# Optimization experiments

Measured on AMD Instinct MI355X. Metric: run time of the kernel, lower is better.

The kernel has to match this reference:

```python
import jax, jax.numpy as jnp
import numpy as np

B, T, N, F = 32, 36, 10000, 3
HORIZON = 10
NUM_REGIONS = 20
NAN_RATE = 0.05


def setup_inputs() -> dict:
    key = jax.random.key(0)
    k1, k2, k3 = jax.random.split(key, 3)
    seq = jax.random.normal(k1, (B, T, N, F), dtype=jnp.float32)
    nan_mask = jax.random.uniform(k2, (B, T, N, F)) < NAN_RATE
    seq = jnp.where(nan_mask, jnp.nan, seq)
    cluster_id = jax.random.randint(k3, (N,), 0, NUM_REGIONS, dtype=jnp.int64)
    return {"seq": seq, "cluster_id": cluster_id}


def _nanmean_all(x):
    valid = ~jnp.isnan(x)
    s = jnp.where(valid, x, 0.0).sum()
    c = valid.sum().astype(x.dtype)
    return s / c


def reference(seq, cluster_id):
    x = seq[..., 0]                               # [B, T, N] speed channel
    valid = ~jnp.isnan(x)
    xz = jnp.where(valid, x, 0.0)
    cnt = valid.sum(axis=1).astype(x.dtype)       # [B, N]
    time_mean = xz.sum(axis=1) / cnt              # [B, N]; NaN if a node is all-NaN
    pred_speed = jnp.tile(time_mean[:, None, :], (1, HORIZON, 1))  # [B, 10, N]

    # per-region nanmean over nodes: segment-mean via one-hot contraction
    onehot = (cluster_id[:, None] == jnp.arange(NUM_REGIONS)).astype(x.dtype)  # [N, R]
    pvalid = ~jnp.isnan(pred_speed)
    pz = jnp.where(pvalid, pred_speed, 0.0)
    rsum = jnp.einsum('bhn,nr->bhr', pz, onehot)                     # [B, 10, R]
    rcnt = jnp.einsum('bhn,nr->bhr', pvalid.astype(x.dtype), onehot)  # [B, 10, R]
    regional = rsum / rcnt                                            # NaN if region all-NaN

    # nan_to_global_avg: replace remaining NaNs with global nanmean of each tensor
    g1 = _nanmean_all(pred_speed)
    g2 = _nanmean_all(regional)
    out_pred = jnp.where(jnp.isnan(pred_speed), g1, pred_speed)
    out_regional = jnp.where(jnp.isnan(regional), g2, regional)
    return out_pred, out_regional
```

## Files before the change

kernel.cpp:

```cpp
#include <hip/hip_runtime.h>

#define BB 32
#define TT 36
#define NN 10000
#define FF 3
#define HH 10
#define RR 20
#define NQ (NN / 4)


__global__ __launch_bounds__(256) void k_time_mean(
        const float* __restrict__ seq,
        const int* __restrict__ cid,
        float* __restrict__ tm,
        float* __restrict__ rsum,
        float* __restrict__ rcnt) {
    __shared__ float ls[RR];
    __shared__ float lc[RR];
    const int b = blockIdx.y;
    const int q = blockIdx.x * blockDim.x + threadIdx.x;
    if (threadIdx.x < RR) { ls[threadIdx.x] = 0.f; lc[threadIdx.x] = 0.f; }
    __syncthreads();

    if (q < NQ) {
        const float4* p = (const float4*)seq + (size_t)b * TT * NN * FF / 4 + 3 * q;
        const size_t tstride = (size_t)NN * FF / 4;
        float s0 = 0.f, s1 = 0.f, s2 = 0.f, s3 = 0.f;
        int c0 = 0, c1 = 0, c2 = 0, c3 = 0;
        #pragma unroll
        for (int t = 0; t < TT; ++t) {
            float4 q0 = p[0];
            float4 q1 = p[1];
            float4 q2 = p[2];
            p += tstride;
            float v0 = q0.x, v1 = q0.w, v2 = q1.z, v3 = q2.y;
            if (v0 == v0) { s0 += v0; c0++; }
            if (v1 == v1) { s1 += v1; c1++; }
            if (v2 == v2) { s2 += v2; c2++; }
            if (v3 == v3) { s3 += v3; c3++; }
        }
        const float nanf_ = __int_as_float(0x7fc00000);
        float m0 = c0 ? s0 / (float)c0 : nanf_;
        float m1 = c1 ? s1 / (float)c1 : nanf_;
        float m2 = c2 ? s2 / (float)c2 : nanf_;
        float m3 = c3 ? s3 / (float)c3 : nanf_;
        ((float4*)tm)[(size_t)b * NQ + q] = make_float4(m0, m1, m2, m3);

        const int4 r4 = ((const int4*)cid)[q];
        if (c0) { atomicAdd(&ls[r4.x], m0); atomicAdd(&lc[r4.x], 1.f); }
        if (c1) { atomicAdd(&ls[r4.y], m1); atomicAdd(&lc[r4.y], 1.f); }
        if (c2) { atomicAdd(&ls[r4.z], m2); atomicAdd(&lc[r4.z], 1.f); }
        if (c3) { atomicAdd(&ls[r4.w], m3); atomicAdd(&lc[r4.w], 1.f); }
    }

    __syncthreads();
    if (threadIdx.x < RR) {
        atomicAdd(&rsum[b * RR + threadIdx.x], ls[threadIdx.x]);
        atomicAdd(&rcnt[b * RR + threadIdx.x], lc[threadIdx.x]);
    }
}

__global__ void k_regional(const float* __restrict__ rsum,
                           const float* __restrict__ rcnt,
                           float* __restrict__ g1out,
                           float* __restrict__ out_reg) {
    const int tid = threadIdx.x;
    __shared__ float sv[10], sc[10], ss[10], sn[10];
    __shared__ float g2s;

    float myrs = 0.f, myrc = 0.f;
    float val = 0.f;
    int valid = 0;
    if (tid < BB * RR) {
        myrs = rsum[tid];
        myrc = rcnt[tid];
        if (myrc > 0.f) { val = myrs / myrc; valid = 1; }
    }

    float wv = valid ? val : 0.f;
    float wc = (float)valid;
    float ws = myrs;
    float wn = myrc;
    for (int off = 32; off > 0; off >>= 1) {
        wv += __shfl_down(wv, off, 64);
        wc += __shfl_down(wc, off, 64);
        ws += __shfl_down(ws, off, 64);
        wn += __shfl_down(wn, off, 64);
    }
    const int wave = tid >> 6;
    if ((tid & 63) == 0) { sv[wave] = wv; sc[wave] = wc; ss[wave] = ws; sn[wave] = wn; }
    __syncthreads();

    if (tid == 0) {
        float v = 0.f, c = 0.f, s = 0.f, n = 0.f;
        #pragma unroll
        for (int i = 0; i < 10; ++i) { v += sv[i]; c += sc[i]; s += ss[i]; n += sn[i]; }
        g2s = v / c;
        g1out[0] = s / n;
    }
    __syncthreads();

    if (tid < BB * RR) {
        const int b = tid / RR, r = tid % RR;
        const float o = valid ? val : g2s;
        #pragma unroll
        for (int h = 0; h < HH; ++h)
            out_reg[(size_t)(b * HH + h) * RR + r] = o;
    }
}

__global__ __launch_bounds__(256) void k_pred(
        const float* __restrict__ tm,
        const float* __restrict__ g1p,
        float* __restrict__ out) {
    const int b = blockIdx.y;
    const int q = blockIdx.x * blockDim.x + threadIdx.x;
    if (q >= NQ) return;
    const float g1 = g1p[0];
    float4 v = ((const float4*)tm)[(size_t)b * NQ + q];
    if (!(v.x == v.x)) v.x = g1;
    if (!(v.y == v.y)) v.y = g1;
    if (!(v.z == v.z)) v.z = g1;
    if (!(v.w == v.w)) v.w = g1;
    float4* o = (float4*)out + (size_t)b * HH * NQ + q;
    #pragma unroll
    for (int h = 0; h < HH; ++h)
        o[(size_t)h * NQ] = v;
}

extern "C" void kernel_launch(void* const* d_in, const int* in_sizes, int n_in,
                              void* d_out, int out_size, void* d_ws, size_t ws_size,
                              hipStream_t stream) {
    const float* seq = (const float*)d_in[0];
    const int*   cid = (const int*)d_in[1];
    float* out = (float*)d_out;

    float* ws   = (float*)d_ws;
    float* tm   = ws;
    float* rsum = tm + BB * NN;
    float* rcnt = rsum + BB * RR;
    float* g1   = rcnt + BB * RR;

    hipMemsetAsync(rsum, 0, (size_t)(2 * BB * RR) * sizeof(float), stream);

    dim3 blk(256);
    dim3 grd((NQ + 255) / 256, BB);
    k_time_mean<<<grd, blk, 0, stream>>>(seq, cid, tm, rsum, rcnt);
    k_regional<<<1, 640, 0, stream>>>(rsum, rcnt, g1,
                                      out + (size_t)BB * HH * NN);
    k_pred<<<grd, blk, 0, stream>>>(tm, g1, out);
}
```

Baseline: 214.8 us.

## Write prediction output directly from time-mean kernel and patch NaNs via list

The time-mean kernel now writes the 10-horizon prediction output directly, using nontemporal loads and stores, instead of staging means in a workspace buffer for a second pass. All-NaN nodes are appended to a global list with an atomic counter. A small fixup kernel then overwrites those entries with the global mean once it is known. This removes the intermediate buffer round trip and a full-size re-read, at the cost of global atomics when many nodes are all-NaN.

```diff
diff --git a/kernel.cpp b/kernel.cpp
--- a/kernel.cpp
+++ b/kernel.cpp
@@ -8,13 +8,17 @@
 #define RR 20
 #define NQ (NN / 4)
 
+typedef float v4f __attribute__((ext_vector_type(4)));
+
 
 __global__ __launch_bounds__(256) void k_time_mean(
         const float* __restrict__ seq,
         const int* __restrict__ cid,
-        float* __restrict__ tm,
+        float* __restrict__ out,
         float* __restrict__ rsum,
-        float* __restrict__ rcnt) {
+        float* __restrict__ rcnt,
+        int* __restrict__ nancnt,
+        int* __restrict__ nanlist) {
     __shared__ float ls[RR];
     __shared__ float lc[RR];
     const int b = blockIdx.y;
@@ -23,17 +27,17 @@
     __syncthreads();
 
     if (q < NQ) {
-        const float4* p = (const float4*)seq + (size_t)b * TT * NN * FF / 4 + 3 * q;
+        const v4f* p = (const v4f*)seq + (size_t)b * TT * NN * FF / 4 + 3 * q;
         const size_t tstride = (size_t)NN * FF / 4;
         float s0 = 0.f, s1 = 0.f, s2 = 0.f, s3 = 0.f;
         int c0 = 0, c1 = 0, c2 = 0, c3 = 0;
         #pragma unroll
         for (int t = 0; t < TT; ++t) {
-            float4 q0 = p[0];
-            float4 q1 = p[1];
-            float4 q2 = p[2];
+            v4f a0 = __builtin_nontemporal_load(p);
+            v4f a1 = __builtin_nontemporal_load(p + 1);
+            v4f a2 = __builtin_nontemporal_load(p + 2);
             p += tstride;
-            float v0 = q0.x, v1 = q0.w, v2 = q1.z, v3 = q2.y;
+            float v0 = a0.x, v1 = a0.w, v2 = a1.z, v3 = a2.y;
             if (v0 == v0) { s0 += v0; c0++; }
             if (v1 == v1) { s1 += v1; c1++; }
             if (v2 == v2) { s2 += v2; c2++; }
@@ -44,7 +48,17 @@
         float m1 = c1 ? s1 / (float)c1 : nanf_;
         float m2 = c2 ? s2 / (float)c2 : nanf_;
         float m3 = c3 ? s3 / (float)c3 : nanf_;
-        ((float4*)tm)[(size_t)b * NQ + q] = make_float4(m0, m1, m2, m3);
+
+        v4f mv; mv.x = m0; mv.y = m1; mv.z = m2; mv.w = m3;
+        v4f* o = (v4f*)out + (size_t)b * HH * NQ + q;
+        #pragma unroll
+        for (int h = 0; h < HH; ++h)
+            __builtin_nontemporal_store(mv, o + (size_t)h * NQ);
+
+        if (!c0) { int i = atomicAdd(nancnt, 1); nanlist[i] = b * NN + 4 * q; }
+        if (!c1) { int i = atomicAdd(nancnt, 1); nanlist[i] = b * NN + 4 * q + 1; }
+        if (!c2) { int i = atomicAdd(nancnt, 1); nanlist[i] = b * NN + 4 * q + 2; }
+        if (!c3) { int i = atomicAdd(nancnt, 1); nanlist[i] = b * NN + 4 * q + 3; }
 
         const int4 r4 = ((const int4*)cid)[q];
         if (c0) { atomicAdd(&ls[r4.x], m0); atomicAdd(&lc[r4.x], 1.f); }
@@ -109,23 +123,21 @@
     }
 }
 
-__global__ __launch_bounds__(256) void k_pred(
-        const float* __restrict__ tm,
-        const float* __restrict__ g1p,
-        float* __restrict__ out) {
-    const int b = blockIdx.y;
-    const int q = blockIdx.x * blockDim.x + threadIdx.x;
-    if (q >= NQ) return;
+__global__ void k_fix(const int* __restrict__ nancnt,
+                      const int* __restrict__ nanlist,
+                      const float* __restrict__ g1p,
+                      float* __restrict__ out) {
+    const int cnt = nancnt[0];
     const float g1 = g1p[0];
-    float4 v = ((const float4*)tm)[(size_t)b * NQ + q];
-    if (!(v.x == v.x)) v.x = g1;
-    if (!(v.y == v.y)) v.y = g1;
-    if (!(v.z == v.z)) v.z = g1;
-    if (!(v.w == v.w)) v.w = g1;
-    float4* o = (float4*)out + (size_t)b * HH * NQ + q;
-    #pragma unroll
-    for (int h = 0; h < HH; ++h)
-        o[(size_t)h * NQ] = v;
+    for (int i = blockIdx.x * blockDim.x + threadIdx.x; i < cnt;
+         i += gridDim.x * blockDim.x) {
+        const int bn = nanlist[i];
+        const int b = bn / NN, n = bn % NN;
+        float* o = out + (size_t)b * HH * NN + n;
+        #pragma unroll
+        for (int h = 0; h < HH; ++h)
+            o[(size_t)h * NN] = g1;
+    }
 }
 
 extern "C" void kernel_launch(void* const* d_in, const int* in_sizes, int n_in,
@@ -135,18 +147,20 @@
     const int*   cid = (const int*)d_in[1];
     float* out = (float*)d_out;
 
-    float* ws   = (float*)d_ws;
-    float* tm   = ws;
-    float* rsum = tm + BB * NN;
-    float* rcnt = rsum + BB * RR;
-    float* g1   = rcnt + BB * RR;
+    float* ws      = (float*)d_ws;
+    int*   nancnt  = (int*)ws;
+    float* g1      = ws + 1;
+    float* rsum    = ws + 2;
+    float* rcnt    = rsum + BB * RR;
+    int*   nanlist = (int*)(rcnt + BB * RR);
 
-    hipMemsetAsync(rsum, 0, (size_t)(2 * BB * RR) * sizeof(float), stream);
+    hipMemsetAsync(nancnt, 0, (size_t)(2 + 2 * BB * RR) * sizeof(float), stream);
 
     dim3 blk(256);
     dim3 grd((NQ + 255) / 256, BB);
-    k_time_mean<<<grd, blk, 0, stream>>>(seq, cid, tm, rsum, rcnt);
+    k_time_mean<<<grd, blk, 0, stream>>>(seq, cid, out, rsum, rcnt,
+                                         nancnt, nanlist);
     k_regional<<<1, 640, 0, stream>>>(rsum, rcnt, g1,
                                       out + (size_t)BB * HH * NN);
-    k_pred<<<grd, blk, 0, stream>>>(tm, g1, out);
+    k_fix<<<40, 256, 0, stream>>>(nancnt, nanlist, g1, out);
 }
```

New measurement: 231.6 us. 1.08x slower.
